# Kernel tuning notes

Hardware: AMD Instinct MI355X
Metric: run time of the kernel (lower is better)

The kernel has to match this reference:

```python
import jax, jax.numpy as jnp
import numpy as np

B = 2; QD = 128; H = QD; W = QD; NQ = QD * QD
EMBED = 256; HEADS = 8; POINTS = 4; D = EMBED // HEADS; FFN = 512


def setup_inputs() -> dict:
    key = jax.random.key(0)
    ks = jax.random.split(key, 16)
    s = 0.02
    rn = lambda k, shp: jax.random.normal(k, shp, jnp.float32) * s
    return {
        'q': jax.random.normal(ks[0], (B, NQ, EMBED), jnp.float32),
        'W_off': rn(ks[1], (EMBED, HEADS * POINTS * 2)),
        'b_off': rn(ks[2], (HEADS * POINTS * 2,)),
        'W_attn': rn(ks[3], (EMBED, HEADS * POINTS)),
        'b_attn': rn(ks[4], (HEADS * POINTS,)),
        'W_val': rn(ks[5], (EMBED, EMBED)),
        'b_val': rn(ks[6], (EMBED,)),
        'W_out': rn(ks[7], (EMBED, EMBED)),
        'b_out': rn(ks[8], (EMBED,)),
        'W1': rn(ks[9], (EMBED, FFN)),
        'b1': rn(ks[10], (FFN,)),
        'W2': rn(ks[11], (FFN, EMBED)),
        'b2': rn(ks[12], (EMBED,)),
        'gamma': jnp.ones((EMBED,), jnp.float32),
        'beta': jnp.zeros((EMBED,), jnp.float32),
    }


def _layernorm(x, g, b):
    m = x.mean(-1, keepdims=True)
    v = ((x - m) ** 2).mean(-1, keepdims=True)
    return (x - m) * jax.lax.rsqrt(v + 1e-5) * g + b


def _msda(q, W_off, b_off, W_attn, b_attn, W_val, b_val, W_out, b_out):
    # value projection; value == query here. (B, NQ, EMBED)
    value = q @ W_val + b_val
    v = value.reshape(B, NQ, HEADS, D).transpose(0, 2, 1, 3)  # (B, heads, Nv, D)

    off = (q @ W_off + b_off).reshape(B, NQ, HEADS, POINTS, 2)
    aw = jax.nn.softmax((q @ W_attn + b_attn).reshape(B, NQ, HEADS, POINTS), axis=-1)

    # reference points: torch.meshgrid(linspace, linspace, indexing='xy')
    lin = jnp.linspace(0.0, 1.0, QD)
    gx, gy = jnp.meshgrid(lin, lin, indexing='xy')
    ref = jnp.stack([gx, gy], -1).reshape(1, NQ, 1, 1, 2)

    # offset_normalizer = [W, H]; sampling locations in [0,1]
    loc = ref + off / jnp.array([W, H], jnp.float32)
    # grid_sample bilinear, align_corners=False: pixel = loc * size - 0.5
    px = (loc[..., 0] * W - 0.5).transpose(0, 2, 1, 3)  # (B, heads, NQ, P)
    py = (loc[..., 1] * H - 0.5).transpose(0, 2, 1, 3)

    x0 = jnp.floor(px)
    y0 = jnp.floor(py)
    sampled = jnp.zeros((B, HEADS, NQ, POINTS, D), jnp.float32)
    for dy in (0.0, 1.0):
        for dx in (0.0, 1.0):
            xi = x0 + dx
            yi = y0 + dy
            wgt = (1.0 - jnp.abs(px - xi)) * (1.0 - jnp.abs(py - yi))
            valid = ((xi >= 0) & (xi <= W - 1) & (yi >= 0) & (yi <= H - 1)).astype(jnp.float32)
            idx = (jnp.clip(yi, 0, H - 1).astype(jnp.int32) * W
                   + jnp.clip(xi, 0, W - 1).astype(jnp.int32))  # (B, heads, NQ, P)
            g = jnp.take_along_axis(v, idx.reshape(B, HEADS, NQ * POINTS, 1), axis=2)
            g = g.reshape(B, HEADS, NQ, POINTS, D)
            sampled = sampled + g * (wgt * valid)[..., None]

    awt = aw.transpose(0, 2, 1, 3)  # (B, heads, NQ, P)
    out = (sampled * awt[..., None]).sum(3)  # (B, heads, NQ, D)
    out = out.transpose(0, 2, 1, 3).reshape(B, NQ, EMBED)
    # mmcv: dropout(output_proj(out)) + identity ; dropout is identity at eval
    return out @ W_out + b_out + q


def reference(q, W_off, b_off, W_attn, b_attn, W_val, b_val, W_out, b_out,
              W1, b1, W2, b2, gamma, beta):
    attn = _msda(q, W_off, b_off, W_attn, b_attn, W_val, b_val, W_out, b_out)
    x = attn + q  # outer residual in the module (in addition to mmcv's internal one)
    ffn = _layernorm(jax.nn.relu(x @ W1 + b1) @ W2 + b2, gamma, beta)
    return x + ffn
```

## Files before the change

kernel.cpp:

```cpp
#include <hip/hip_runtime.h>
#include <hip/hip_bf16.h>
#include <cstddef>
#include <cstdint>

#define B_      2
#define QD_     128
#define NQ_     (QD_ * QD_)
#define EMBED_  256
#define HEADS_  8
#define POINTS_ 4
#define FFN_    512
#define RTOT_   (B_ * NQ_)
#define NCATP_  384

using bf16x8 = __attribute__((ext_vector_type(8))) short;
using f32x4  = __attribute__((ext_vector_type(4))) float;

__device__ __forceinline__ short f2bf(float f) {
    unsigned u = __float_as_uint(f);
    u += 0x7FFFu + ((u >> 16) & 1u);
    return (short)(u >> 16);
}
__device__ __forceinline__ float bf2f(short s) {
    return __uint_as_float(((unsigned)(unsigned short)s) << 16);
}

#define GLDS(gp, lp) __builtin_amdgcn_global_load_lds( \
        (const __attribute__((address_space(1))) void*)(gp), \
        (__attribute__((address_space(3))) void*)(lp), 16, 0, 0)

#define WCAT_ELEMS  (NCATP_ * 256)
#define WOUT_ELEMS  (256 * 256)
#define W1_ELEMS    (512 * 256)
#define W2_ELEMS    (256 * 512)
#define WCAT_BLOCKS ((WCAT_ELEMS + 255) / 256)
#define SAMP_BLOCKS (RTOT_ / 8)
#define PREP2_ELEMS (WOUT_ELEMS + W1_ELEMS + W2_ELEMS)
#define PREP2_BLOCKS ((PREP2_ELEMS + 255) / 256)

__global__ __launch_bounds__(256) void prep_wcat(
        const float* __restrict__ Wv, const float* __restrict__ Wo,
        const float* __restrict__ Wa, const float* __restrict__ bv,
        const float* __restrict__ bo, const float* __restrict__ ba,
        short* __restrict__ WcatT, float* __restrict__ bcat) {
    int idx = blockIdx.x * 256 + threadIdx.x;
    if (idx < WCAT_ELEMS) {
        int c = idx >> 8, k = idx & 255;
        float v = 0.f;
        if (c < 256)      v = Wv[k * 256 + c];
        else if (c < 320) v = Wo[k * 64 + (c - 256)];
        else if (c < 352) v = Wa[k * 32 + (c - 320)];
        WcatT[idx] = f2bf(v);
    }
    if (idx < NCATP_) {
        float v = 0.f;
        if (idx < 256)      v = bv[idx];
        else if (idx < 320) v = bo[idx - 256];
        else if (idx < 352) v = ba[idx - 320];
        bcat[idx] = v;
    }
}

__global__ __launch_bounds__(512) void gemm1_fused(
        const float* __restrict__ q,
        const short* __restrict__ WcatT,
        const float* __restrict__ bcat,
        short* __restrict__ vcomp,
        float* __restrict__ pm) {
    __shared__ __align__(16) short xs[128 * 256];
    __shared__ __align__(16) short Bs[2][128 * 64];

    const int t    = threadIdx.x;
    const int ln   = t & 63;
    const int w    = t >> 6;
    const int wr   = w >> 2;
    const int wc   = w & 3;
    const int lrow = ln & 15;
    const int lkg  = ln >> 4;
    const int row0 = blockIdx.x * 128;
    const int orow = lkg * 4;
    const int ocol = lrow;

    auto stage_b = [&](int step, int buf) {
        const int p  = step >> 2;
        const int kt = step & 3;
        #pragma unroll
        for (int j = 0; j < 2; ++j) {
            const int c0 = (w * 2 + j) * 64;
            const int c  = c0 + ln;
            const int r  = c >> 3;
            const int s  = (c & 7) ^ (r & 7);
            GLDS(WcatT + (size_t)(p * 128 + r) * 256 + kt * 64 + s * 8,
                 &Bs[buf][c0 * 8]);
        }
    };

    stage_b(0, 0);
    #pragma unroll
    for (int j = 0; j < 8; ++j) {
        const int c = t + 512 * j;
        const int r = c >> 5;
        const int s = c & 31;
        const float* qp = q + (size_t)(row0 + r) * 256 + s * 8;
        const float4 f0 = *(const float4*)qp;
        const float4 f1 = *(const float4*)(qp + 4);
        bf16x8 v;
        v[0] = f2bf(f0.x); v[1] = f2bf(f0.y); v[2] = f2bf(f0.z); v[3] = f2bf(f0.w);
        v[4] = f2bf(f1.x); v[5] = f2bf(f1.y); v[6] = f2bf(f1.z); v[7] = f2bf(f1.w);
        const int kt = s >> 3, sc = s & 7;
        *(bf16x8*)&xs[kt * 8192 + r * 64 + (sc ^ (r & 7)) * 8] = v;
    }
    __syncthreads();

    f32x4 acc[4][2] = {};
    const f32x4 zero = {0.f, 0.f, 0.f, 0.f};

    int buf = 0;
    #pragma unroll 1
    for (int step = 0; step < 12; ++step) {
        if (step < 11) stage_b(step + 1, buf ^ 1);
        const int kt = step & 3;
        #pragma unroll
        for (int ks = 0; ks < 2; ++ks) {
            const int slot = ((ks * 4 + lkg) ^ (lrow & 7)) * 8;
            bf16x8 af[4], bfr[2];
            #pragma unroll
            for (int m = 0; m < 4; ++m)
                af[m] = *(const bf16x8*)&xs[kt * 8192 + (wr * 64 + m * 16 + lrow) * 64 + slot];
            #pragma unroll
            for (int n = 0; n < 2; ++n)
                bfr[n] = *(const bf16x8*)&Bs[buf][(wc * 32 + n * 16 + lrow) * 64 + slot];
            #pragma unroll
            for (int m = 0; m < 4; ++m)
                #pragma unroll
                for (int n = 0; n < 2; ++n)
                    acc[m][n] = __builtin_amdgcn_mfma_f32_16x16x32_bf16(
                        af[m], bfr[n], acc[m][n], 0, 0, 0);
        }
        __syncthreads();
        if ((step & 3) == 3) {
            const int p = step >> 2;
            #pragma unroll
            for (int m = 0; m < 4; ++m) {
                #pragma unroll
                for (int n = 0; n < 2; ++n) {
                    const int gcol = p * 128 + wc * 32 + n * 16 + ocol;
                    const float bv = bcat[gcol];
                    #pragma unroll
                    for (int rr = 0; rr < 4; ++rr) {
                        const int row = wr * 64 + m * 16 + orow + rr;
                        const float v = acc[m][n][rr] + bv;
                        if (gcol < 256) {
                            vcomp[(size_t)(row0 + row) * 256 + gcol] = f2bf(v);
                        } else {
                            const int cc = gcol - 256;
                            if (cc < 96)
                                pm[(size_t)(row0 + row) * 128 + cc] = v;
                        }
                    }
                    acc[m][n] = zero;
                }
            }
        }
        buf ^= 1;
    }
}

__global__ __launch_bounds__(256) void msda_sample(
        const float* __restrict__ pm, const short* __restrict__ vcomp,
        short* __restrict__ msda,
        const float* __restrict__ W_out, const float* __restrict__ W1,
        const float* __restrict__ W2,
        short* __restrict__ WoutT, short* __restrict__ W1T,
        short* __restrict__ W2T) {
    if (blockIdx.x >= SAMP_BLOCKS) {
        int idx = (blockIdx.x - SAMP_BLOCKS) * 256 + threadIdx.x;
        if (idx < WOUT_ELEMS) {
            int c = idx >> 8, k = idx & 255;
            WoutT[idx] = f2bf(W_out[k * 256 + c]);
        } else if (idx < WOUT_ELEMS + W1_ELEMS) {
            int j = idx - WOUT_ELEMS; int c = j >> 8, k = j & 255;
            W1T[j] = f2bf(W1[k * 512 + c]);
        } else if (idx < PREP2_ELEMS) {
            int j = idx - (WOUT_ELEMS + W1_ELEMS); int c = j >> 9, k = j & 511;
            W2T[j] = f2bf(W2[k * 256 + c]);
        }
        return;
    }

    __shared__ int   s_off[8][32][4];
    __shared__ float s_c[8][32][4];

    const int t  = threadIdx.x;
    const int r0 = blockIdx.x * 8;
    const int bq = r0 >> 14;

    {
        const int g = t >> 5, cmb = t & 31, h = cmb >> 2, p = cmb & 3;
        const int r = r0 + g;
        const int n = r & (NQ_ - 1);
        const int gi = n >> 7, gj = n & 127;
        const float* pr = pm + (size_t)r * 128;

        const float l0 = pr[64 + h * 4 + 0], l1 = pr[64 + h * 4 + 1];
        const float l2 = pr[64 + h * 4 + 2], l3 = pr[64 + h * 4 + 3];
        const float mx = fmaxf(fmaxf(l0, l1), fmaxf(l2, l3));
        const float sum = expf(l0 - mx) + expf(l1 - mx) + expf(l2 - mx) + expf(l3 - mx);
        const float lp = pr[64 + h * 4 + p];
        const float aw = expf(lp - mx) / sum;

        const float ox = pr[h * 8 + p * 2 + 0];
        const float oy = pr[h * 8 + p * 2 + 1];
        const float px = (gj * (1.0f / 127.0f) + ox * (1.0f / 128.0f)) * 128.0f - 0.5f;
        const float py = (gi * (1.0f / 127.0f) + oy * (1.0f / 128.0f)) * 128.0f - 0.5f;
        const float x0f = floorf(px), y0f = floorf(py);
        const int   x0 = (int)x0f, y0 = (int)y0f;
        const float fx = px - x0f, fy = py - y0f;
        const int x0c = min(max(x0, 0), 127), x1c = min(max(x0 + 1, 0), 127);
        const int y0c = min(max(y0, 0), 127), y1c = min(max(y0 + 1, 0), 127);
        const float vx0 = ((unsigned)x0 <= 127u) ? 1.f : 0.f;
        const float vx1 = ((unsigned)(x0 + 1) <= 127u) ? 1.f : 0.f;
        const float vy0 = ((unsigned)y0 <= 127u) ? 1.f : 0.f;
        const float vy1 = ((unsigned)(y0 + 1) <= 127u) ? 1.f : 0.f;

        s_off[g][cmb][0] = (y0c * 128 + x0c) * 512;
        s_off[g][cmb][1] = (y0c * 128 + x1c) * 512;
        s_off[g][cmb][2] = (y1c * 128 + x0c) * 512;
        s_off[g][cmb][3] = (y1c * 128 + x1c) * 512;
        s_c[g][cmb][0] = aw * (1.f - fx) * (1.f - fy) * vx0 * vy0;
        s_c[g][cmb][1] = aw * fx * (1.f - fy) * vx1 * vy0;
        s_c[g][cmb][2] = aw * (1.f - fx) * fy * vx0 * vy1;
        s_c[g][cmb][3] = aw * fx * fy * vx1 * vy1;
    }
    __syncthreads();

    const int half = t >> 7;
    const int h    = (t >> 4) & 7;
    const int dd   = t & 15;
    const char* vb = (const char*)vcomp + ((size_t)bq * NQ_ * 256 + h * 32 + dd * 2) * 2;

    #pragma unroll
    for (int it = 0; it < 4; ++it) {
        const int g = it * 2 + half;
        float a0 = 0.f, a1 = 0.f;
        #pragma unroll
        for (int p = 0; p < 4; ++p) {
            const int cmb = h * 4 + p;
            #pragma unroll
            for (int k = 0; k < 4; ++k) {
                const unsigned u = *(const unsigned*)(vb + s_off[g][cmb][k]);
                const float c = s_c[g][cmb][k];
                a0 += c * __uint_as_float(u << 16);
                a1 += c * __uint_as_float(u & 0xffff0000u);
            }
        }
        const int r = r0 + g;
        const unsigned o = (unsigned)(unsigned short)f2bf(a0)
                         | ((unsigned)(unsigned short)f2bf(a1) << 16);
        *(unsigned*)&msda[(size_t)r * 256 + h * 32 + dd * 2] = o;
    }
}

__global__ __launch_bounds__(512) void gemm_x_ffn1(
        const short* __restrict__ msda,
        const short* __restrict__ WoutT,
        const float* __restrict__ b_out,
        const float* __restrict__ qf,
        const short* __restrict__ W1T,
        const float* __restrict__ b1,
        short* __restrict__ xbf,
        short* __restrict__ hid) {
    __shared__ __align__(16) short xs[128 * 256];
    __shared__ __align__(16) short stg[128 * 192];
    short* As = stg;
    short* Bs = stg + 128 * 64;

    const int t    = threadIdx.x;
    const int ln   = t & 63;
    const int w    = t >> 6;
    const int wr   = w >> 2;
    const int wc   = w & 3;
    const int lrow = ln & 15;
    const int lkg  = ln >> 4;
    const int row0 = blockIdx.x * 128;
    const int orow = lkg * 4;
    const int ocol = lrow;

    f32x4 acc[4][4] = {};
    for (int kt = 0; kt < 4; ++kt) {
        #pragma unroll
        for (int j = 0; j < 2; ++j) {
            const int c0 = (w * 2 + j) * 64;
            const int cc = c0 + ln;
            const int r  = cc >> 3;
            const int s  = (cc & 7) ^ (r & 7);
            GLDS(msda + (size_t)(row0 + r) * 256 + kt * 64 + s * 8, &As[c0 * 8]);
        }
        #pragma unroll
        for (int j = 0; j < 4; ++j) {
            const int c0 = (w * 4 + j) * 64;
            const int cc = c0 + ln;
            const int r  = cc >> 3;
            const int s  = (cc & 7) ^ (r & 7);
            GLDS(WoutT + (size_t)r * 256 + kt * 64 + s * 8, &Bs[c0 * 8]);
        }
        __syncthreads();
        #pragma unroll
        for (int ks = 0; ks < 2; ++ks) {
            const int slot = ((ks * 4 + lkg) ^ (lrow & 7)) * 8;
            bf16x8 af[4], bfr[4];
            #pragma unroll
            for (int m = 0; m < 4; ++m)
                af[m] = *(const bf16x8*)&As[(wr * 64 + m * 16 + lrow) * 64 + slot];
            #pragma unroll
            for (int n = 0; n < 4; ++n)
                bfr[n] = *(const bf16x8*)&Bs[(wc * 64 + n * 16 + lrow) * 64 + slot];
            #pragma unroll
            for (int m = 0; m < 4; ++m)
                #pragma unroll
                for (int n = 0; n < 4; ++n)
                    acc[m][n] = __builtin_amdgcn_mfma_f32_16x16x32_bf16(
                        af[m], bfr[n], acc[m][n], 0, 0, 0);
        }
        __syncthreads();
    }

    #pragma unroll
    for (int m = 0; m < 4; ++m) {
        #pragma unroll
        for (int n = 0; n < 4; ++n) {
            const int kk  = n * 16 + ocol;
            const int col = wc * 64 + kk;
            const float bv = b_out[col];
            #pragma unroll
            for (int rr = 0; rr < 4; ++rr) {
                const int row = wr * 64 + m * 16 + orow + rr;
                float v = acc[m][n][rr] + bv
                        + 2.f * qf[(size_t)(row0 + row) * 256 + col];
                const short bb = f2bf(v);
                xbf[(size_t)(row0 + row) * 256 + col] = bb;
                xs[wc * 8192 + row * 64 + ((kk >> 3) ^ (row & 7)) * 8 + (kk & 7)] = bb;
            }
        }
    }
    __syncthreads();

    #pragma unroll 1
    for (int p = 0; p < 2; ++p) {
        f32x4 acc2[4][4] = {};
        for (int kt = 0; kt < 4; ++kt) {
            #pragma unroll
            for (int j = 0; j < 4; ++j) {
                const int c0 = (w * 4 + j) * 64;
                const int cc = c0 + ln;
                const int r  = cc >> 3;
                const int s  = (cc & 7) ^ (r & 7);
                GLDS(W1T + (size_t)(p * 256 + r) * 256 + kt * 64 + s * 8, &Bs[c0 * 8]);
            }
            __syncthreads();
            #pragma unroll
            for (int ks = 0; ks < 2; ++ks) {
                const int slot = ((ks * 4 + lkg) ^ (lrow & 7)) * 8;
                bf16x8 af[4], bfr[4];
                #pragma unroll
                for (int m = 0; m < 4; ++m)
                    af[m] = *(const bf16x8*)&xs[kt * 8192 + (wr * 64 + m * 16 + lrow) * 64 + slot];
                #pragma unroll
                for (int n = 0; n < 4; ++n)
                    bfr[n] = *(const bf16x8*)&Bs[(wc * 64 + n * 16 + lrow) * 64 + slot];
                #pragma unroll
                for (int m = 0; m < 4; ++m)
                    #pragma unroll
                    for (int n = 0; n < 4; ++n)
                        acc2[m][n] = __builtin_amdgcn_mfma_f32_16x16x32_bf16(
                            af[m], bfr[n], acc2[m][n], 0, 0, 0);
            }
            __syncthreads();
        }
        #pragma unroll
        for (int m = 0; m < 4; ++m) {
            #pragma unroll
            for (int n = 0; n < 4; ++n) {
                const int col = p * 256 + wc * 64 + n * 16 + ocol;
                const float bv = b1[col];
                #pragma unroll
                for (int rr = 0; rr < 4; ++rr) {
                    const int row = wr * 64 + m * 16 + orow + rr;
                    hid[(size_t)(row0 + row) * 512 + col] =
                        f2bf(fmaxf(acc2[m][n][rr] + bv, 0.f));
                }
            }
        }
    }
}

__global__ __launch_bounds__(256) void gemm_ln(
        const short* __restrict__ A,
        const short* __restrict__ Bt,
        const float* __restrict__ bias,
        const short* __restrict__ xres,
        const float* __restrict__ gamma, const float* __restrict__ beta,
        float* __restrict__ out, int M, int K) {
    __shared__ __align__(16) short As[2][64 * 64];
    __shared__ __align__(16) short Bs[256 * 64];
    __shared__ float red[64][4][2];

    const int t    = threadIdx.x;
    const int ln   = t & 63;
    const int w    = t >> 6;
    const int lrow = ln & 15;
    const int lkg  = ln >> 4;
    const int row0 = blockIdx.x * 64;

    f32x4 acc[4][4] = {};

    auto stage_a = [&](int buf, int k0) {
        #pragma unroll
        for (int j = 0; j < 2; ++j) {
            const int c0 = (w * 2 + j) * 64;
            const int c  = c0 + ln;
            const int r  = c >> 3;
            const int s  = (c & 7) ^ (r & 7);
            GLDS(A + (size_t)(row0 + r) * K + (k0 + s * 8), &As[buf][c0 * 8]);
        }
    };
    auto stage_b = [&](int k0) {
        #pragma unroll
        for (int j = 0; j < 8; ++j) {
            const int c0 = (w * 8 + j) * 64;
            const int c  = c0 + ln;
            const int r  = c >> 3;
            const int s  = (c & 7) ^ (r & 7);
            GLDS(Bt + (size_t)r * K + (k0 + s * 8), &Bs[c0 * 8]);
        }
    };

    stage_a(0, 0);
    stage_b(0);
    __syncthreads();
    int buf = 0;
    for (int kt = 0; kt < 8; ++kt) {
        if (kt < 7) stage_a(buf ^ 1, kt * 64 + 64);
        #pragma unroll
        for (int ks = 0; ks < 2; ++ks) {
            const int slot = ((ks * 4 + lkg) ^ (lrow & 7)) * 8;
            bf16x8 af[4], bfr[4];
            #pragma unroll
            for (int m = 0; m < 4; ++m)
                af[m] = *(const bf16x8*)&As[buf][(m * 16 + lrow) * 64 + slot];
            #pragma unroll
            for (int n = 0; n < 4; ++n)
                bfr[n] = *(const bf16x8*)&Bs[(w * 64 + n * 16 + lrow) * 64 + slot];
            #pragma unroll
            for (int m = 0; m < 4; ++m)
                #pragma unroll
                for (int n = 0; n < 4; ++n)
                    acc[m][n] = __builtin_amdgcn_mfma_f32_16x16x32_bf16(
                        af[m], bfr[n], acc[m][n], 0, 0, 0);
        }
        __syncthreads();
        if (kt < 7) {
            stage_b(kt * 64 + 64);
            __syncthreads();
        }
        buf ^= 1;
    }

    const int orow = lkg * 4;
    const int ocol = lrow;

    #pragma unroll
    for (int n = 0; n < 4; ++n) {
        const float bv = bias[w * 64 + n * 16 + ocol];
        #pragma unroll
        for (int m = 0; m < 4; ++m)
            #pragma unroll
            for (int rr = 0; rr < 4; ++rr)
                acc[m][n][rr] += bv;
    }

    #pragma unroll
    for (int m = 0; m < 4; ++m) {
        #pragma unroll
        for (int rr = 0; rr < 4; ++rr) {
            float s = 0.f, sq = 0.f;
            #pragma unroll
            for (int n = 0; n < 4; ++n) {
                const float v = acc[m][n][rr];
                s += v; sq += v * v;
            }
            #pragma unroll
            for (int o = 1; o < 16; o <<= 1) {
                s  += __shfl_xor(s, o, 64);
                sq += __shfl_xor(sq, o, 64);
            }
            if (ocol == 0) {
                const int row = m * 16 + orow + rr;
                red[row][w][0] = s;
                red[row][w][1] = sq;
            }
        }
    }
    __syncthreads();

    #pragma unroll
    for (int m = 0; m < 4; ++m) {
        #pragma unroll
        for (int rr = 0; rr < 4; ++rr) {
            const int row = m * 16 + orow + rr;
            const float S  = red[row][0][0] + red[row][1][0] + red[row][2][0] + red[row][3][0];
            const float SQ = red[row][0][1] + red[row][1][1] + red[row][2][1] + red[row][3][1];
            const float mean = S * (1.0f / 256.0f);
            const float var  = SQ * (1.0f / 256.0f) - mean * mean;
            const float rs   = rsqrtf(var + 1e-5f);
            const size_t rbase = (size_t)(row0 + row) * 256;
            #pragma unroll
            for (int n = 0; n < 4; ++n) {
                const int col = w * 64 + n * 16 + ocol;
                out[rbase + col] = bf2f(xres[rbase + col])
                                 + (acc[m][n][rr] - mean) * rs * gamma[col] + beta[col];
            }
        }
    }
}

extern "C" void kernel_launch(void* const* d_in, const int* in_sizes, int n_in,
                              void* d_out, int out_size, void* d_ws, size_t ws_size,
                              hipStream_t stream) {
    const float* q      = (const float*)d_in[0];
    const float* b_out  = (const float*)d_in[8];
    const float* b1     = (const float*)d_in[10];
    const float* b2     = (const float*)d_in[12];
    const float* gamma  = (const float*)d_in[13];
    const float* beta   = (const float*)d_in[14];

    float* out = (float*)d_out;

    char* w = (char*)d_ws;
    float* pm    = (float*)w; w += (size_t)RTOT_ * 128 * 4;
    short* vcomp = (short*)w; w += (size_t)RTOT_ * 256 * 2;
    short* msda  = (short*)w; w += (size_t)RTOT_ * EMBED_ * 2;
    short* xbf   = (short*)w; w += (size_t)RTOT_ * EMBED_ * 2;
    short* hid   = (short*)w; w += (size_t)RTOT_ * FFN_ * 2;
    short* WcatT = (short*)w; w += WCAT_ELEMS * 2;
    short* WoutT = (short*)w; w += WOUT_ELEMS * 2;
    short* W1T   = (short*)w; w += W1_ELEMS * 2;
    short* W2T   = (short*)w; w += W2_ELEMS * 2;
    float* bcat  = (float*)w; w += NCATP_ * 4;

    prep_wcat<<<WCAT_BLOCKS, 256, 0, stream>>>(
        (const float*)d_in[5], (const float*)d_in[1], (const float*)d_in[3],
        (const float*)d_in[6], (const float*)d_in[2], (const float*)d_in[4],
        WcatT, bcat);

    gemm1_fused<<<RTOT_ / 128, 512, 0, stream>>>(
        q, WcatT, bcat, vcomp, pm);

    msda_sample<<<SAMP_BLOCKS + PREP2_BLOCKS, 256, 0, stream>>>(
        pm, vcomp, msda,
        (const float*)d_in[7], (const float*)d_in[9], (const float*)d_in[11],
        WoutT, W1T, W2T);

    gemm_x_ffn1<<<RTOT_ / 128, 512, 0, stream>>>(
        msda, WoutT, b_out, q, W1T, b1, xbf, hid);

    gemm_ln<<<RTOT_ / 64, 256, 0, stream>>>(
        hid, W2T, b2, xbf, gamma, beta, out, RTOT_, FFN_);
}
```

Before: 102.7 us.

## Double-buffer weight tiles and preload activations in fused output-proj/FFN1 kernel

Restructures gemm_x_ffn1 so all four msda K-tiles are loaded into LDS up front, and the weight tiles (WoutT, then W1T) are double-buffered. The next tile's global-to-LDS load is issued before computing the current one, removing one barrier per K step and overlapping memory with MFMA work. The first W1T tile is prefetched during the epilogue that writes xbf/xs. Separately, the pm buffer stride shrinks from 128 to 96 floats, cutting its memory footprint and traffic. LDS use rises to 128 KB per block, which may limit occupancy.

```diff
diff --git a/kernel.cpp b/kernel.cpp
--- a/kernel.cpp
+++ b/kernel.cpp
@@ -12,6 +12,7 @@
 #define FFN_    512
 #define RTOT_   (B_ * NQ_)
 #define NCATP_  384
+#define PMW_    96
 
 using bf16x8 = __attribute__((ext_vector_type(8))) short;
 using f32x4  = __attribute__((ext_vector_type(4))) float;
@@ -154,8 +155,8 @@
                             vcomp[(size_t)(row0 + row) * 256 + gcol] = f2bf(v);
                         } else {
                             const int cc = gcol - 256;
-                            if (cc < 96)
-                                pm[(size_t)(row0 + row) * 128 + cc] = v;
+                            if (cc < PMW_)
+                                pm[(size_t)(row0 + row) * PMW_ + cc] = v;
                         }
                     }
                     acc[m][n] = zero;
@@ -200,7 +201,7 @@
         const int r = r0 + g;
         const int n = r & (NQ_ - 1);
         const int gi = n >> 7, gj = n & 127;
-        const float* pr = pm + (size_t)r * 128;
+        const float* pr = pm + (size_t)r * PMW_;
 
         const float l0 = pr[64 + h * 4 + 0], l1 = pr[64 + h * 4 + 1];
         const float l2 = pr[64 + h * 4 + 2], l3 = pr[64 + h * 4 + 3];
@@ -270,10 +271,8 @@
         const float* __restrict__ b1,
         short* __restrict__ xbf,
         short* __restrict__ hid) {
-    __shared__ __align__(16) short xs[128 * 256];
-    __shared__ __align__(16) short stg[128 * 192];
-    short* As = stg;
-    short* Bs = stg + 128 * 64;
+    __shared__ __align__(16) short xs[4][128 * 64];
+    __shared__ __align__(16) short Bs[2][256 * 64];
 
     const int t    = threadIdx.x;
     const int ln   = t & 63;
@@ -286,35 +285,47 @@
     const int orow = lkg * 4;
     const int ocol = lrow;
 
-    f32x4 acc[4][4] = {};
-    for (int kt = 0; kt < 4; ++kt) {
-        #pragma unroll
-        for (int j = 0; j < 2; ++j) {
-            const int c0 = (w * 2 + j) * 64;
-            const int cc = c0 + ln;
-            const int r  = cc >> 3;
-            const int s  = (cc & 7) ^ (r & 7);
-            GLDS(msda + (size_t)(row0 + r) * 256 + kt * 64 + s * 8, &As[c0 * 8]);
-        }
+    auto stage_msda = [&]() {
+        #pragma unroll
+        for (int j = 0; j < 8; ++j) {
+            const int kt = j >> 1;
+            const int c0 = (w * 2 + (j & 1)) * 64;
+            const int c  = c0 + ln;
+            const int r  = c >> 3;
+            const int s  = (c & 7) ^ (r & 7);
+            GLDS(msda + (size_t)(row0 + r) * 256 + kt * 64 + s * 8, &xs[kt][c0 * 8]);
+        }
+    };
+    auto stage_w = [&](const short* W, int roff, int kt, int buf) {
         #pragma unroll
         for (int j = 0; j < 4; ++j) {
             const int c0 = (w * 4 + j) * 64;
-            const int cc = c0 + ln;
-            const int r  = cc >> 3;
-            const int s  = (cc & 7) ^ (r & 7);
-            GLDS(WoutT + (size_t)r * 256 + kt * 64 + s * 8, &Bs[c0 * 8]);
-        }
-        __syncthreads();
+            const int c  = c0 + ln;
+            const int r  = c >> 3;
+            const int s  = (c & 7) ^ (r & 7);
+            GLDS(W + (size_t)(roff + r) * 256 + kt * 64 + s * 8, &Bs[buf][c0 * 8]);
+        }
+    };
+
+    stage_msda();
+    stage_w(WoutT, 0, 0, 0);
+    __syncthreads();
+
+    f32x4 acc[4][4] = {};
+    int buf = 0;
+    #pragma unroll 1
+    for (int kt = 0; kt < 4; ++kt) {
+        if (kt < 3) stage_w(WoutT, 0, kt + 1, buf ^ 1);
         #pragma unroll
         for (int ks = 0; ks < 2; ++ks) {
             const int slot = ((ks * 4 + lkg) ^ (lrow & 7)) * 8;
             bf16x8 af[4], bfr[4];
             #pragma unroll
             for (int m = 0; m < 4; ++m)
-                af[m] = *(const bf16x8*)&As[(wr * 64 + m * 16 + lrow) * 64 + slot];
+                af[m] = *(const bf16x8*)&xs[kt][(wr * 64 + m * 16 + lrow) * 64 + slot];
             #pragma unroll
             for (int n = 0; n < 4; ++n)
-                bfr[n] = *(const bf16x8*)&Bs[(wc * 64 + n * 16 + lrow) * 64 + slot];
+                bfr[n] = *(const bf16x8*)&Bs[buf][(wc * 64 + n * 16 + lrow) * 64 + slot];
             #pragma unroll
             for (int m = 0; m < 4; ++m)
                 #pragma unroll
@@ -323,7 +334,10 @@
                         af[m], bfr[n], acc[m][n], 0, 0, 0);
         }
         __syncthreads();
-    }
+        buf ^= 1;
+    }
+
+    stage_w(W1T, 0, 0, 0);
 
     #pragma unroll
     for (int m = 0; m < 4; ++m) {
@@ -339,35 +353,31 @@
                         + 2.f * qf[(size_t)(row0 + row) * 256 + col];
                 const short bb = f2bf(v);
                 xbf[(size_t)(row0 + row) * 256 + col] = bb;
-                xs[wc * 8192 + row * 64 + ((kk >> 3) ^ (row & 7)) * 8 + (kk & 7)] = bb;
+                xs[wc][row * 64 + ((kk >> 3) ^ (row & 7)) * 8 + (kk & 7)] = bb;
             }
         }
     }
     __syncthreads();
 
+    int buf2 = 0;
     #pragma unroll 1
     for (int p = 0; p < 2; ++p) {
         f32x4 acc2[4][4] = {};
+        #pragma unroll 1
         for (int kt = 0; kt < 4; ++kt) {
-            #pragma unroll
-            for (int j = 0; j < 4; ++j) {
-                const int c0 = (w * 4 + j) * 64;
-                const int cc = c0 + ln;
-                const int r  = cc >> 3;
-                const int s  = (cc & 7) ^ (r & 7);
-                GLDS(W1T + (size_t)(p * 256 + r) * 256 + kt * 64 + s * 8, &Bs[c0 * 8]);
-            }
-            __syncthreads();
+            const int nstep = p * 4 + kt + 1;
+            if (nstep < 8)
+                stage_w(W1T, (nstep >> 2) * 256, nstep & 3, buf2 ^ 1);
             #pragma unroll
             for (int ks = 0; ks < 2; ++ks) {
                 const int slot = ((ks * 4 + lkg) ^ (lrow & 7)) * 8;
                 bf16x8 af[4], bfr[4];
                 #pragma unroll
                 for (int m = 0; m < 4; ++m)
-                    af[m] = *(const bf16x8*)&xs[kt * 8192 + (wr * 64 + m * 16 + lrow) * 64 + slot];
+                    af[m] = *(const bf16x8*)&xs[kt][(wr * 64 + m * 16 + lrow) * 64 + slot];
                 #pragma unroll
                 for (int n = 0; n < 4; ++n)
-                    bfr[n] = *(const bf16x8*)&Bs[(wc * 64 + n * 16 + lrow) * 64 + slot];
+                    bfr[n] = *(const bf16x8*)&Bs[buf2][(wc * 64 + n * 16 + lrow) * 64 + slot];
                 #pragma unroll
                 for (int m = 0; m < 4; ++m)
                     #pragma unroll
@@ -376,6 +386,7 @@
                             af[m], bfr[n], acc2[m][n], 0, 0, 0);
             }
             __syncthreads();
+            buf2 ^= 1;
         }
         #pragma unroll
         for (int m = 0; m < 4; ++m) {
@@ -537,7 +548,7 @@
     float* out = (float*)d_out;
 
     char* w = (char*)d_ws;
-    float* pm    = (float*)w; w += (size_t)RTOT_ * 128 * 4;
+    float* pm    = (float*)w; w += (size_t)RTOT_ * PMW_ * 4;
     short* vcomp = (short*)w; w += (size_t)RTOT_ * 256 * 2;
     short* msda  = (short*)w; w += (size_t)RTOT_ * EMBED_ * 2;
     short* xbf   = (short*)w; w += (size_t)RTOT_ * EMBED_ * 2;
```

After: 102.3 us. No clear change (-0.4%).
